# Kernel optimization log

Measured on AMD Instinct MI355X. Metric: run time of the kernel, lower is better.

The kernel has to match this reference:

```python
import jax, jax.numpy as jnp
import numpy as np

N_BASIS = 128   # n_atom_basis F
N_INT   = 3     # n_interactions
N_RBF   = 20
CUTOFF  = 5.0
MAX_Z   = 100
EPS     = 1e-8
N_ATOMS = 25000
N_EDGES = 200000


def setup_inputs() -> dict:
    key = jax.random.key(0)
    ks = jax.random.split(key, 16)
    F = N_BASIS
    s = 0.02
    z     = jax.random.randint(ks[0], (N_ATOMS,), 1, MAX_Z)
    pos   = jax.random.uniform(ks[1], (N_ATOMS, 3), dtype=jnp.float32) * 2.0  # small box -> inside cutoff
    idx_i = jax.random.randint(ks[2], (N_EDGES,), 0, N_ATOMS)
    idx_j = jax.random.randint(ks[3], (N_EDGES,), 0, N_ATOMS)
    emb   = jax.random.normal(ks[4], (MAX_Z, F), dtype=jnp.float32) * s
    fW    = jax.random.normal(ks[5], (N_RBF, 3 * F * N_INT), dtype=jnp.float32) * s
    fb    = jnp.zeros((3 * F * N_INT,), jnp.float32)
    iW1   = jax.random.normal(ks[6], (N_INT, F, F), dtype=jnp.float32) * s
    ib1   = jnp.zeros((N_INT, F), jnp.float32)
    iW2   = jax.random.normal(ks[7], (N_INT, F, 3 * F), dtype=jnp.float32) * s
    ib2   = jnp.zeros((N_INT, 3 * F), jnp.float32)
    mWmix = jax.random.normal(ks[8], (N_INT, F, 2 * F), dtype=jnp.float32) * s
    mW1   = jax.random.normal(ks[9], (N_INT, 2 * F, F), dtype=jnp.float32) * s
    mb1   = jnp.zeros((N_INT, F), jnp.float32)
    mW2   = jax.random.normal(ks[10], (N_INT, F, 3 * F), dtype=jnp.float32) * s
    mb2   = jnp.zeros((N_INT, 3 * F), jnp.float32)
    return dict(z=z, pos=pos, idx_i=idx_i, idx_j=idx_j, emb=emb, fW=fW, fb=fb,
                iW1=iW1, ib1=ib1, iW2=iW2, ib2=ib2,
                mWmix=mWmix, mW1=mW1, mb1=mb1, mW2=mW2, mb2=mb2)


def reference(z, pos, idx_i, idx_j, emb, fW, fb, iW1, ib1, iW2, ib2,
              mWmix, mW1, mb1, mW2, mb2):
    F = N_BASIS
    n_atoms = z.shape[0]
    # geometry
    r_ij = pos[idx_j] - pos[idx_i]                                  # [E,3]
    r_ij = jnp.where(jnp.abs(r_ij) < 1e-6, 1e-6, r_ij)
    d_ij = jnp.linalg.norm(r_ij, axis=1, keepdims=True)             # [E,1]
    dir_ij = r_ij / d_ij                                            # [E,3]
    # Gaussian radial basis
    offsets = jnp.linspace(0.0, CUTOFF, N_RBF)
    width = offsets[1] - offsets[0]
    coeff = -0.5 / (width * width)
    phi = jnp.exp(coeff * (d_ij[..., None] - offsets) ** 2)         # [E,1,n_rbf]
    # cosine cutoff
    fcut = 0.5 * (jnp.cos(jnp.pi * d_ij / CUTOFF) + 1.0) * (d_ij < CUTOFF)  # [E,1]
    filters = (phi @ fW + fb) * fcut[..., None]                     # [E,1,3F*I]
    filter_list = jnp.split(filters, N_INT, axis=-1)                # each [E,1,3F]
    # initial atom features
    q = emb[z][:, None, :]                                          # [N,1,F]
    mu = jnp.zeros((n_atoms, 3, F), q.dtype)                        # [N,3,F]
    for t in range(N_INT):
        # --- interaction (gather - filter-multiply - scatter-add) ---
        x = jax.nn.silu(q @ iW1[t] + ib1[t]) @ iW2[t] + ib2[t]      # [N,1,3F]
        xj = x[idx_j]                                               # [E,1,3F]
        muj = mu[idx_j]                                             # [E,3,F]
        x = filter_list[t] * xj                                     # [E,1,3F]
        dq, dmuR, dmumu = jnp.split(x, 3, axis=-1)                  # [E,1,F] each
        dq = jax.ops.segment_sum(dq, idx_i, num_segments=n_atoms)   # [N,1,F]
        dmu = dmuR * dir_ij[..., None] + dmumu * muj                # [E,3,F]
        dmu = jax.ops.segment_sum(dmu, idx_i, num_segments=n_atoms) # [N,3,F]
        q = q + dq
        mu = mu + dmu
        # --- mixing (intra-atomic) ---
        mu_mix = mu @ mWmix[t]                                      # [N,3,2F]
        mu_V, mu_W = jnp.split(mu_mix, 2, axis=-1)                  # [N,3,F]
        mu_Vn = jnp.sqrt(jnp.sum(mu_V ** 2, axis=-2, keepdims=True) + EPS)  # [N,1,F]
        ctx = jnp.concatenate([q, mu_Vn], axis=-1)                  # [N,1,2F]
        x = jax.nn.silu(ctx @ mW1[t] + mb1[t]) @ mW2[t] + mb2[t]    # [N,1,3F]
        dq_intra, dmu_intra, dqmu_intra = jnp.split(x, 3, axis=-1)
        dmu_intra = dmu_intra * mu_W                                # [N,3,F]
        dqmu_intra = dqmu_intra * jnp.sum(mu_V * mu_W, axis=1, keepdims=True)
        q = q + dq_intra + dqmu_intra
        mu = mu + dmu_intra
    return q.squeeze(1), mu
```

## Files before the change

kernel.cpp:

```cpp
#include <hip/hip_runtime.h>
#include <hip/hip_bf16.h>

#define F 128
#define F3 384
#define NRBF 20
#define NITER 3
#define KP 24

typedef __hip_bfloat16 bf16;
typedef __bf16 bfrag __attribute__((ext_vector_type(8)));
typedef float f32x4 __attribute__((ext_vector_type(4)));

__device__ __forceinline__ float b2f(bf16 v) { return __bfloat162float(v); }
__device__ __forceinline__ bf16 f2b(float v) { return __float2bfloat16(v); }
__device__ __forceinline__ bfrag ldb(const bf16* p) { return *(const bfrag*)p; }
__device__ __forceinline__ bfrag ldsb(const __bf16* p) { return *(const bfrag*)p; }
__device__ __forceinline__ bfrag cvtf(const float* p) {
    bfrag r;
#pragma unroll
    for (int j = 0; j < 8; ++j) r[j] = (__bf16)p[j];
    return r;
}

__global__ void detect_kernel(const unsigned short* __restrict__ raw, int n_u16,
                              int* __restrict__ flag) {
    int i = blockIdx.x * blockDim.x + threadIdx.x;
    int bad = 0;
    for (int k = i; k < n_u16; k += blockDim.x * gridDim.x) {
        unsigned e = (raw[k] >> 7) & 0xFFu;
        if (e >= 140u) bad = 1;
    }
    if (bad) atomicOr(flag, 1);
}

struct CvtArgs {
    const void* src[13];
    float* dst[13];
    int end[14];
};
__global__ void cvt_all_kernel(CvtArgs a, const int* __restrict__ flag, int total) {
    int idx = blockIdx.x * blockDim.x + threadIdx.x;
    if (idx >= total) return;
    int s = 0;
    while (idx >= a.end[s + 1]) ++s;
    int local = idx - a.end[s];
    float v = (*flag) ? ((const float*)a.src[s])[local]
                      : b2f(((const bf16*)a.src[s])[local]);
    a.dst[s][local] = v;
}

struct TpArgs {
    const float* src[5];
    bf16* dst[5];
    int K[5];
    int Nn[5];
    int end[6];
};
__global__ void tpose_all_kernel(TpArgs a, int total) {
    int idx = blockIdx.x * blockDim.x + threadIdx.x;
    if (idx >= total) return;
    int s = 0;
    while (idx >= a.end[s + 1]) ++s;
    int local = idx - a.end[s];
    int K = a.K[s], Nn = a.Nn[s], slice = K * Nn;
    int t = local / slice, j = local - t * slice;
    int n = j / K, k = j - n * K;
    a.dst[s][local] = f2b(a.src[s][t * slice + k * Nn + n]);
}

__global__ void fwt_kernel(const float* __restrict__ fW, const float* __restrict__ fb,
                           float* __restrict__ dst, int total) {
    int idx = blockIdx.x * blockDim.x + threadIdx.x;
    if (idx >= total) return;
    int k = idx % KP, rest = idx / KP;
    int n = rest % F3, t = rest / F3;
    float v = (k < NRBF) ? fW[k * (F3 * NITER) + t * F3 + n]
                         : (k == NRBF ? fb[t * F3 + n] : 0.0f);
    dst[idx] = v;
}

__global__ void geom_kernel(const float* __restrict__ pos, const int* __restrict__ ii,
                            const int* __restrict__ jj, const int* __restrict__ rank,
                            bf16* __restrict__ phifc2, float* __restrict__ dir2, int E) {
    int e = blockIdx.x * blockDim.x + threadIdx.x;
    if (e >= E) return;
    int i = ii[e], j = jj[e], l = rank[e];
    float r[3];
#pragma unroll
    for (int d = 0; d < 3; ++d) {
        float v = pos[j * 3 + d] - pos[i * 3 + d];
        if (fabsf(v) < 1e-6f) v = 1e-6f;
        r[d] = v;
    }
    float dd = sqrtf(r[0] * r[0] + r[1] * r[1] + r[2] * r[2]);
    float inv = 1.0f / dd;
#pragma unroll
    for (int d = 0; d < 3; ++d) dir2[(size_t)l * 4 + d] = r[d] * inv;
    dir2[(size_t)l * 4 + 3] = __int_as_float(j);
    const float CUT = 5.0f;
    const float PI = 3.14159265358979323846f;
    float fc = (dd < CUT) ? 0.5f * (cosf(PI * dd / CUT) + 1.0f) : 0.0f;
    const float width = CUT / (NRBF - 1);
    const float coeff = -0.5f / (width * width);
    bf16* pr = phifc2 + (size_t)l * KP;
#pragma unroll
    for (int k = 0; k < NRBF; ++k) {
        float diff = dd - (float)k * width;
        pr[k] = f2b(expf(coeff * diff * diff) * fc);
    }
    pr[NRBF] = f2b(fc);
    pr[NRBF + 1] = f2b(0.0f);
    pr[NRBF + 2] = f2b(0.0f);
    pr[NRBF + 3] = f2b(0.0f);
}

__global__ void embed_kernel(const int* __restrict__ z, const float* __restrict__ emb,
                             float* __restrict__ q, int N) {
    int idx = blockIdx.x * blockDim.x + threadIdx.x;
    if (idx >= N * F) return;
    int n = idx >> 7, f = idx & 127;
    q[idx] = emb[z[n] * F + f];
}

__global__ void count_kernel(const int* __restrict__ ii, int* __restrict__ counts, int E) {
    int e = blockIdx.x * blockDim.x + threadIdx.x;
    if (e < E) atomicAdd(&counts[ii[e]], 1);
}

__global__ void scan_kernel(const int* __restrict__ counts, int* __restrict__ offs, int N) {
    __shared__ int cum[1024];
    int t = threadIdx.x;
    int chunk = (N + 1023) >> 10;
    int b = t * chunk;
    int e = b + chunk; if (e > N) e = N;
    int s = 0;
    for (int a = b; a < e; ++a) s += counts[a];
    cum[t] = s;
    __syncthreads();
    for (int o = 1; o < 1024; o <<= 1) {
        int u = (t >= o) ? cum[t - o] : 0;
        __syncthreads();
        cum[t] += u;
        __syncthreads();
    }
    int run = cum[t] - s;
    for (int a = b; a < e; ++a) { offs[a] = run; run += counts[a]; }
    if (t == 1023) offs[N] = cum[1023];
}

__global__ void fill_kernel(const int* __restrict__ ii, const int* __restrict__ offs,
                            int* __restrict__ cursor, int* __restrict__ rank, int E) {
    int e = blockIdx.x * blockDim.x + threadIdx.x;
    if (e >= E) return;
    int i = ii[e];
    int p = atomicAdd(&cursor[i], 1);
    rank[e] = offs[i] + p;
}

__global__ __launch_bounds__(256) void atom_x_mfma(
    const float* __restrict__ q, const bf16* __restrict__ W1T, const float* __restrict__ b1,
    const bf16* __restrict__ W2T, const float* __restrict__ b2, bf16* __restrict__ x, int N) {
    __shared__ __bf16 H[32][136];
    int tid = threadIdx.x;
    int w = tid >> 6, l = tid & 63;
    int lm = l & 15, q4 = l >> 4;
    int i0 = blockIdx.x * 32;
    f32x4 acc[2][2] = {};
    int r0 = min(i0 + lm, N - 1);
    int r1 = min(i0 + 16 + lm, N - 1);
    for (int kt = 0; kt < 4; ++kt) {
        int ko = kt * 32 + q4 * 8;
        bfrag a0 = cvtf(q + (size_t)r0 * F + ko);
        bfrag a1 = cvtf(q + (size_t)r1 * F + ko);
        bfrag b0 = ldb(W1T + (size_t)(w * 32 + lm) * F + ko);
        bfrag b1f = ldb(W1T + (size_t)(w * 32 + 16 + lm) * F + ko);
        acc[0][0] = __builtin_amdgcn_mfma_f32_16x16x32_bf16(a0, b0, acc[0][0], 0, 0, 0);
        acc[1][0] = __builtin_amdgcn_mfma_f32_16x16x32_bf16(a1, b0, acc[1][0], 0, 0, 0);
        acc[0][1] = __builtin_amdgcn_mfma_f32_16x16x32_bf16(a0, b1f, acc[0][1], 0, 0, 0);
        acc[1][1] = __builtin_amdgcn_mfma_f32_16x16x32_bf16(a1, b1f, acc[1][1], 0, 0, 0);
    }
#pragma unroll
    for (int nt = 0; nt < 2; ++nt) {
        int col = w * 32 + nt * 16 + lm;
        float bb = b1[col];
#pragma unroll
        for (int mt = 0; mt < 2; ++mt)
#pragma unroll
            for (int r = 0; r < 4; ++r) {
                float v = acc[mt][nt][r] + bb;
                H[mt * 16 + q4 * 4 + r][col] = (__bf16)(v / (1.0f + expf(-v)));
            }
    }
    __syncthreads();
#pragma unroll
    for (int j = 0; j < 6; ++j) {
        int n0 = w * 96 + j * 16;
        f32x4 c0 = {}, c1 = {};
        const bf16* bp = W2T + (size_t)(n0 + lm) * F;
        for (int kt = 0; kt < 4; ++kt) {
            int ko = kt * 32 + q4 * 8;
            bfrag a0 = ldsb(&H[lm][ko]);
            bfrag a1 = ldsb(&H[16 + lm][ko]);
            bfrag bf = ldb(bp + ko);
            c0 = __builtin_amdgcn_mfma_f32_16x16x32_bf16(a0, bf, c0, 0, 0, 0);
            c1 = __builtin_amdgcn_mfma_f32_16x16x32_bf16(a1, bf, c1, 0, 0, 0);
        }
        int col = n0 + lm;
        float bb = b2[col];
#pragma unroll
        for (int r = 0; r < 4; ++r) {
            int row0 = i0 + q4 * 4 + r;
            int row1 = row0 + 16;
            if (row0 < N) x[(size_t)row0 * F3 + col] = f2b(c0[r] + bb);
            if (row1 < N) x[(size_t)row1 * F3 + col] = f2b(c1[r] + bb);
        }
    }
}

template<int T0>
__global__ __launch_bounds__(128, 2) void edge_gather_d(
    const bf16* __restrict__ mu_in, const bf16* __restrict__ x,
    const bf16* __restrict__ phifc2, const float* __restrict__ dir2,
    const float* __restrict__ fWTf, const int* __restrict__ offs,
    bf16* __restrict__ dq, bf16* __restrict__ dmu, int N) {
    int i = blockIdx.x;
    int f = threadIdx.x;
    float w0[21], w1[21], w2[21];
    {
        const f32x4* p0 = (const f32x4*)(fWTf + (size_t)f * KP);
        const f32x4* p1 = (const f32x4*)(fWTf + (size_t)(f + 128) * KP);
#pragma unroll
        for (int k = 0; k < 6; ++k) {
            f32x4 t0 = p0[k], t1 = p1[k];
#pragma unroll
            for (int r = 0; r < 4; ++r) {
                int kk = k * 4 + r;
                if (kk < 21) { w0[kk] = t0[r]; w1[kk] = t1[r]; }
            }
        }
        if constexpr (!T0) {
            const f32x4* p2 = (const f32x4*)(fWTf + (size_t)(f + 256) * KP);
#pragma unroll
            for (int k = 0; k < 6; ++k) {
                f32x4 t2 = p2[k];
#pragma unroll
                for (int r = 0; r < 4; ++r) {
                    int kk = k * 4 + r;
                    if (kk < 21) w2[kk] = t2[r];
                }
            }
        }
    }
#pragma unroll
    for (int k = 0; k < 21; ++k) {
        asm volatile("" : "+v"(w0[k]), "+v"(w1[k]));
        if constexpr (!T0) asm volatile("" : "+v"(w2[k]));
    }
    int beg = offs[i], end = offs[i + 1];
    float accq = 0.0f, am0 = 0.0f, am1 = 0.0f, am2 = 0.0f;
    for (int l = beg; l < end; ++l) {
        const bfrag* pb = (const bfrag*)(phifc2 + (size_t)l * KP);
        bfrag p0 = __builtin_nontemporal_load(pb);
        bfrag p1 = __builtin_nontemporal_load(pb + 1);
        bfrag p2 = __builtin_nontemporal_load(pb + 2);
        float ph[21];
#pragma unroll
        for (int k = 0; k < 8; ++k) ph[k] = (float)p0[k];
#pragma unroll
        for (int k = 0; k < 8; ++k) ph[8 + k] = (float)p1[k];
#pragma unroll
        for (int k = 0; k < 5; ++k) ph[16 + k] = (float)p2[k];
        float fl0 = 0.0f, fl1 = 0.0f, fl2 = 0.0f;
#pragma unroll
        for (int k = 0; k < 21; ++k) {
            fl0 += ph[k] * w0[k];
            fl1 += ph[k] * w1[k];
            if constexpr (!T0) fl2 += ph[k] * w2[k];
        }
        f32x4 dv = __builtin_nontemporal_load((const f32x4*)(dir2 + (size_t)l * 4));
        int j = __float_as_int(dv[3]);
        const bf16* xj = x + (size_t)j * F3;
        float dqv = fl0 * b2f(xj[f]);
        float dR = fl1 * b2f(xj[f + 128]);
        accq += dqv;
        if constexpr (!T0) {
            float dM = fl2 * b2f(xj[f + 256]);
            const bf16* muj = mu_in + (size_t)j * F3;
            am0 += dR * dv[0] + dM * b2f(muj[f]);
            am1 += dR * dv[1] + dM * b2f(muj[f + 128]);
            am2 += dR * dv[2] + dM * b2f(muj[f + 256]);
        } else {
            am0 += dR * dv[0];
            am1 += dR * dv[1];
            am2 += dR * dv[2];
        }
    }
    dq[(size_t)i * F + f] = f2b(accq);
    size_t mb = (size_t)i * F3 + f;
    dmu[mb]       = f2b(am0);
    dmu[mb + 128] = f2b(am1);
    dmu[mb + 256] = f2b(am2);
}

template<int T0, int EMITX, int OUT>
__global__ __launch_bounds__(256) void mix_mfma(
    float* __restrict__ q, const bf16* __restrict__ dqb,
    const bf16* __restrict__ mu_in, const bf16* __restrict__ dmu,
    bf16* __restrict__ mu_out,
    const bf16* __restrict__ WmixT, const bf16* __restrict__ W1T, const float* __restrict__ b1,
    const bf16* __restrict__ W2T, const float* __restrict__ b2,
    const bf16* __restrict__ xW1T, const float* __restrict__ xb1,
    const bf16* __restrict__ xW2T, const float* __restrict__ xb2, bf16* __restrict__ xout,
    void* __restrict__ outp, const int* __restrict__ flag, int N) {
    __shared__ __align__(16) char smem[46048];
    __bf16 (*WW)[130] = (__bf16(*)[130])(smem);
    __bf16 (*VV)[131] = (__bf16(*)[131])(smem + 12480);
    __bf16 (*Y)[392]  = (__bf16(*)[392])(smem + 12480);
    __bf16 (*CT)[264] = (__bf16(*)[264])(smem + 25056);
    __bf16 (*HM)[136] = (__bf16(*)[136])(smem + 33504);
    float  (*SS)[128] = (float(*)[128])(smem + 37856);
    int tid = threadIdx.x;
    int w = tid >> 6, l = tid & 63;
    int lm = l & 15, q4 = l >> 4;
    int i0 = blockIdx.x * 16;
    int rowsM = N * 3;
    {
        f32x4 acc[3][4] = {};
        int mr[3];
#pragma unroll
        for (int mt = 0; mt < 3; ++mt) mr[mt] = min(i0 * 3 + mt * 16 + lm, rowsM - 1);
        for (int kt = 0; kt < 4; ++kt) {
            int ko = kt * 32 + q4 * 8;
            bfrag a[3], b[4];
#pragma unroll
            for (int mt = 0; mt < 3; ++mt) {
                bfrag d = ldb(dmu + (size_t)mr[mt] * F + ko);
                if constexpr (T0) {
                    a[mt] = d;
                } else {
                    bfrag u = ldb(mu_in + (size_t)mr[mt] * F + ko);
#pragma unroll
                    for (int jj = 0; jj < 8; ++jj)
                        a[mt][jj] = (__bf16)((float)u[jj] + (float)d[jj]);
                }
            }
#pragma unroll
            for (int nt = 0; nt < 4; ++nt)
                b[nt] = ldb(WmixT + (size_t)(w * 64 + nt * 16 + lm) * F + ko);
#pragma unroll
            for (int mt = 0; mt < 3; ++mt)
#pragma unroll
                for (int nt = 0; nt < 4; ++nt)
                    acc[mt][nt] = __builtin_amdgcn_mfma_f32_16x16x32_bf16(a[mt], b[nt], acc[mt][nt], 0, 0, 0);
        }
#pragma unroll
        for (int mt = 0; mt < 3; ++mt)
#pragma unroll
            for (int nt = 0; nt < 4; ++nt) {
                int col = w * 64 + nt * 16 + lm;
#pragma unroll
                for (int r = 0; r < 4; ++r) {
                    int row = mt * 16 + q4 * 4 + r;
                    if (col < 128) VV[row][col] = (__bf16)acc[mt][nt][r];
                    else           WW[row][col - 128] = (__bf16)acc[mt][nt][r];
                }
            }
    }
    __syncthreads();
    for (int idx = tid; idx < 16 * F; idx += 256) {
        int a = idx >> 7, f = idx & 127;
        int i = min(i0 + a, N - 1);
        float v0 = (float)VV[a * 3 + 0][f], w0 = (float)WW[a * 3 + 0][f];
        float v1 = (float)VV[a * 3 + 1][f], w1 = (float)WW[a * 3 + 1][f];
        float v2 = (float)VV[a * 3 + 2][f], w2 = (float)WW[a * 3 + 2][f];
        SS[a][f] = v0 * w0 + v1 * w1 + v2 * w2;
        float qe = q[(size_t)i * F + f] + b2f(dqb[(size_t)i * F + f]);
        CT[a][f] = (__bf16)qe;
        CT[a][F + f] = (__bf16)sqrtf(v0 * v0 + v1 * v1 + v2 * v2 + 1e-8f);
    }
    __syncthreads();
    {
        f32x4 c[2] = {};
        for (int kt = 0; kt < 8; ++kt) {
            int ko = kt * 32 + q4 * 8;
            bfrag a = ldsb(&CT[lm][ko]);
#pragma unroll
            for (int nt = 0; nt < 2; ++nt) {
                bfrag b = ldb(W1T + (size_t)(w * 32 + nt * 16 + lm) * 256 + ko);
                c[nt] = __builtin_amdgcn_mfma_f32_16x16x32_bf16(a, b, c[nt], 0, 0, 0);
            }
        }
#pragma unroll
        for (int nt = 0; nt < 2; ++nt) {
            int col = w * 32 + nt * 16 + lm;
            float bb = b1[col];
#pragma unroll
            for (int r = 0; r < 4; ++r) {
                float v = c[nt][r] + bb;
                HM[q4 * 4 + r][col] = (__bf16)(v / (1.0f + expf(-v)));
            }
        }
    }
    __syncthreads();
#pragma unroll
    for (int j = 0; j < 6; ++j) {
        int n0 = w * 96 + j * 16;
        f32x4 c = {};
        const bf16* bp = W2T + (size_t)(n0 + lm) * F;
        for (int kt = 0; kt < 4; ++kt) {
            int ko = kt * 32 + q4 * 8;
            bfrag a = ldsb(&HM[lm][ko]);
            bfrag b = ldb(bp + ko);
            c = __builtin_amdgcn_mfma_f32_16x16x32_bf16(a, b, c, 0, 0, 0);
        }
        int col = n0 + lm;
        float bb = b2[col];
#pragma unroll
        for (int r = 0; r < 4; ++r)
            Y[q4 * 4 + r][col] = (__bf16)(c[r] + bb);
    }
    __syncthreads();
    int nq = N * F;
    for (int idx = tid; idx < 16 * F; idx += 256) {
        int a = idx >> 7, f = idx & 127;
        int i = i0 + a;
        if (i >= N) continue;
        float W0 = (float)WW[a * 3 + 0][f];
        float W1v = (float)WW[a * 3 + 1][f];
        float W2v = (float)WW[a * 3 + 2][f];
        float s = SS[a][f];
        float yq = (float)Y[a][f], ym = (float)Y[a][F + f], ys = (float)Y[a][2 * F + f];
        size_t qb = (size_t)i * F + f;
        float qv = q[qb] + b2f(dqb[qb]) + yq + ys * s;
        size_t mb = (size_t)i * F3 + f;
        float m0 = b2f(dmu[mb]);
        float m1 = b2f(dmu[mb + 128]);
        float m2 = b2f(dmu[mb + 256]);
        if constexpr (!T0) {
            m0 += b2f(mu_in[mb]);
            m1 += b2f(mu_in[mb + 128]);
            m2 += b2f(mu_in[mb + 256]);
        }
        m0 += ym * W0;
        m1 += ym * W1v;
        m2 += ym * W2v;
        if constexpr (OUT) {
            if (*flag) {
                float* of = (float*)outp;
                of[qb] = qv;
                of[nq + mb] = m0;
                of[nq + mb + 128] = m1;
                of[nq + mb + 256] = m2;
            } else {
                bf16* ob = (bf16*)outp;
                ob[qb] = f2b(qv);
                ob[nq + mb] = f2b(m0);
                ob[nq + mb + 128] = f2b(m1);
                ob[nq + mb + 256] = f2b(m2);
            }
        } else {
            q[qb] = qv;
            mu_out[mb]       = f2b(m0);
            mu_out[mb + 128] = f2b(m1);
            mu_out[mb + 256] = f2b(m2);
        }
        if constexpr (EMITX) CT[a][f] = (__bf16)qv;
    }
    if constexpr (EMITX) {
        __syncthreads();
        {
            f32x4 c[2] = {};
            for (int kt = 0; kt < 4; ++kt) {
                int ko = kt * 32 + q4 * 8;
                bfrag a = ldsb(&CT[lm][ko]);
#pragma unroll
                for (int nt = 0; nt < 2; ++nt) {
                    bfrag b = ldb(xW1T + (size_t)(w * 32 + nt * 16 + lm) * F + ko);
                    c[nt] = __builtin_amdgcn_mfma_f32_16x16x32_bf16(a, b, c[nt], 0, 0, 0);
                }
            }
#pragma unroll
            for (int nt = 0; nt < 2; ++nt) {
                int col = w * 32 + nt * 16 + lm;
                float bb = xb1[col];
#pragma unroll
                for (int r = 0; r < 4; ++r) {
                    float v = c[nt][r] + bb;
                    HM[q4 * 4 + r][col] = (__bf16)(v / (1.0f + expf(-v)));
                }
            }
        }
        __syncthreads();
#pragma unroll
        for (int j = 0; j < 6; ++j) {
            int n0 = w * 96 + j * 16;
            f32x4 c = {};
            const bf16* bp = xW2T + (size_t)(n0 + lm) * F;
            for (int kt = 0; kt < 4; ++kt) {
                int ko = kt * 32 + q4 * 8;
                bfrag a = ldsb(&HM[lm][ko]);
                bfrag b = ldb(bp + ko);
                c = __builtin_amdgcn_mfma_f32_16x16x32_bf16(a, b, c, 0, 0, 0);
            }
            int col = n0 + lm;
            float bb = xb2[col];
#pragma unroll
            for (int r = 0; r < 4; ++r) {
                int row = i0 + q4 * 4 + r;
                if (row < N) xout[(size_t)row * F3 + col] = f2b(c[r] + bb);
            }
        }
    }
}

extern "C" void kernel_launch(void* const* d_in, const int* in_sizes, int n_in,
                              void* d_out, int out_size, void* d_ws, size_t ws_size,
                              hipStream_t stream) {
    const int* z = (const int*)d_in[0];
    const int* idx_i = (const int*)d_in[2];
    const int* idx_j = (const int*)d_in[3];

    int N = in_sizes[0];
    int E = in_sizes[2];

    char* base = (char*)d_ws;
    size_t off = 0;
    auto alloc = [&](size_t bytes) -> void* {
        void* p = base + off;
        off += (bytes + 255) & ~(size_t)255;
        return p;
    };

    int* flag = (int*)alloc(4);
    float* pos_f = (float*)alloc((size_t)in_sizes[1] * 4);
    float* emb_f = (float*)alloc((size_t)in_sizes[4] * 4);
    float* fW_f = (float*)alloc((size_t)in_sizes[5] * 4);
    float* fb_f = (float*)alloc((size_t)in_sizes[6] * 4);
    float* iW1_f = (float*)alloc((size_t)in_sizes[7] * 4);
    float* ib1_f = (float*)alloc((size_t)in_sizes[8] * 4);
    float* iW2_f = (float*)alloc((size_t)in_sizes[9] * 4);
    float* ib2_f = (float*)alloc((size_t)in_sizes[10] * 4);
    float* mWmix_f = (float*)alloc((size_t)in_sizes[11] * 4);
    float* mW1_f = (float*)alloc((size_t)in_sizes[12] * 4);
    float* mb1_f = (float*)alloc((size_t)in_sizes[13] * 4);
    float* mW2_f = (float*)alloc((size_t)in_sizes[14] * 4);
    float* mb2_f = (float*)alloc((size_t)in_sizes[15] * 4);
    bf16* iW1T = (bf16*)alloc((size_t)NITER * F * F * 2);
    bf16* iW2T = (bf16*)alloc((size_t)NITER * F3 * F * 2);
    bf16* mWmixT = (bf16*)alloc((size_t)NITER * 2 * F * F * 2);
    bf16* mW1T = (bf16*)alloc((size_t)NITER * F * 2 * F * 2);
    bf16* mW2T = (bf16*)alloc((size_t)NITER * F3 * F * 2);
    float* fWTf = (float*)alloc((size_t)NITER * F3 * KP * 4);
    float* q = (float*)alloc((size_t)N * F * 4);
    bf16* dqb = (bf16*)alloc((size_t)N * F * 2);
    bf16* mua = (bf16*)alloc((size_t)N * F3 * 2);
    bf16* mub = (bf16*)alloc((size_t)N * F3 * 2);
    bf16* dmub = (bf16*)alloc((size_t)N * F3 * 2);
    bf16* xbuf = (bf16*)alloc((size_t)N * F3 * 2);
    bf16* phifc2 = (bf16*)alloc((size_t)(E + 16) * KP * 2);
    float* dir2 = (float*)alloc((size_t)(E + 16) * 4 * 4);
    int* rank = (int*)alloc((size_t)E * 4);
    int* counts = (int*)alloc((size_t)N * 4);
    int* offs = (int*)alloc((size_t)(N + 1) * 4);

    hipMemsetAsync(flag, 0, 4, stream);
    detect_kernel<<<64, 256, 0, stream>>>((const unsigned short*)d_in[1], in_sizes[1], flag);

    {
        CvtArgs a;
        const int srcIdx[13] = {1, 4, 5, 6, 7, 8, 9, 10, 11, 12, 13, 14, 15};
        float* dsts[13] = {pos_f, emb_f, fW_f, fb_f, iW1_f, ib1_f, iW2_f, ib2_f,
                           mWmix_f, mW1_f, mb1_f, mW2_f, mb2_f};
        int cum = 0;
        a.end[0] = 0;
        for (int s = 0; s < 13; ++s) {
            a.src[s] = d_in[srcIdx[s]];
            a.dst[s] = dsts[s];
            cum += in_sizes[srcIdx[s]];
            a.end[s + 1] = cum;
        }
        cvt_all_kernel<<<(cum + 255) / 256, 256, 0, stream>>>(a, flag, cum);
    }

    {
        TpArgs a;
        const float* srcs[5] = {iW1_f, iW2_f, mWmix_f, mW1_f, mW2_f};
        bf16* dsts[5] = {iW1T, iW2T, mWmixT, mW1T, mW2T};
        int Ks[5] = {F, F, F, 2 * F, F};
        int Nns[5] = {F, F3, 2 * F, F, F3};
        int cum = 0;
        a.end[0] = 0;
        for (int s = 0; s < 5; ++s) {
            a.src[s] = srcs[s];
            a.dst[s] = dsts[s];
            a.K[s] = Ks[s];
            a.Nn[s] = Nns[s];
            cum += NITER * Ks[s] * Nns[s];
            a.end[s + 1] = cum;
        }
        tpose_all_kernel<<<(cum + 255) / 256, 256, 0, stream>>>(a, cum);
    }
    {
        int total = NITER * F3 * KP;
        fwt_kernel<<<(total + 255) / 256, 256, 0, stream>>>(fW_f, fb_f, fWTf, total);
    }

    hipMemsetAsync(counts, 0, (size_t)N * 4, stream);
    count_kernel<<<(E + 255) / 256, 256, 0, stream>>>(idx_i, counts, E);
    scan_kernel<<<1, 1024, 0, stream>>>(counts, offs, N);
    hipMemsetAsync(counts, 0, (size_t)N * 4, stream);
    fill_kernel<<<(E + 255) / 256, 256, 0, stream>>>(idx_i, offs, counts, rank, E);

    geom_kernel<<<(E + 255) / 256, 256, 0, stream>>>(pos_f, idx_i, idx_j, rank,
                                                     phifc2, dir2, E);
    embed_kernel<<<(N * F + 255) / 256, 256, 0, stream>>>(z, emb_f, q, N);

    int mixGrid = (N + 15) / 16;
    bf16* muin = mua;
    bf16* muout = mub;
    atom_x_mfma<<<(N + 31) / 32, 256, 0, stream>>>(q, iW1T, ib1_f, iW2T, ib2_f, xbuf, N);
    edge_gather_d<1><<<N, 128, 0, stream>>>(muin, xbuf, phifc2, dir2,
                                            fWTf, offs, dqb, dmub, N);
    mix_mfma<1, 1, 0><<<mixGrid, 256, 0, stream>>>(q, dqb, muin, dmub, muout,
                                                   mWmixT, mW1T, mb1_f, mW2T, mb2_f,
                                                   iW1T + (size_t)1 * F * F, ib1_f + 1 * F,
                                                   iW2T + (size_t)1 * F3 * F, ib2_f + 1 * F3,
                                                   xbuf, nullptr, flag, N);
    { bf16* tm = muin; muin = muout; muout = tm; }
    edge_gather_d<0><<<N, 128, 0, stream>>>(muin, xbuf, phifc2, dir2,
                                            fWTf + (size_t)1 * F3 * KP, offs, dqb, dmub, N);
    mix_mfma<0, 1, 0><<<mixGrid, 256, 0, stream>>>(q, dqb, muin, dmub, muout,
                                                   mWmixT + (size_t)1 * 2 * F * F,
                                                   mW1T + (size_t)1 * F * 2 * F, mb1_f + 1 * F,
                                                   mW2T + (size_t)1 * F3 * F, mb2_f + 1 * F3,
                                                   iW1T + (size_t)2 * F * F, ib1_f + 2 * F,
                                                   iW2T + (size_t)2 * F3 * F, ib2_f + 2 * F3,
                                                   xbuf, nullptr, flag, N);
    { bf16* tm = muin; muin = muout; muout = tm; }
    edge_gather_d<0><<<N, 128, 0, stream>>>(muin, xbuf, phifc2, dir2,
                                            fWTf + (size_t)2 * F3 * KP, offs, dqb, dmub, N);
    mix_mfma<0, 0, 1><<<mixGrid, 256, 0, stream>>>(q, dqb, muin, dmub, muout,
                                                   mWmixT + (size_t)2 * 2 * F * F,
                                                   mW1T + (size_t)2 * F * 2 * F, mb1_f + 2 * F,
                                                   mW2T + (size_t)2 * F3 * F, mb2_f + 2 * F3,
                                                   nullptr, nullptr, nullptr, nullptr,
                                                   nullptr, d_out, flag, N);
}
```

Baseline: 761.2 us.

## Split fused mixing kernel into separate mix, context-MLP and atom-x kernels

Breaks the monolithic mixing kernel into three launches: one computes the mixed mu_V/mu_W products and writes the norm, dot product and mu_W to global buffers; one runs the context MLP and final update on 32-atom tiles; and the existing atom_x kernel computes the next interaction's x. The goal is to cut shared-memory use and register pressure for higher occupancy, and to reuse each weight fragment across two row tiles in the MLP. The cost is extra global traffic for the intermediate buffers (Vn, S, W) and more kernel launches.

```diff
diff --git a/kernel.cpp b/kernel.cpp
--- a/kernel.cpp
+++ b/kernel.cpp
@@ -302,23 +302,13 @@
     dmu[mb + 256] = f2b(am2);
 }
 
-template<int T0, int EMITX, int OUT>
-__global__ __launch_bounds__(256) void mix_mfma(
-    float* __restrict__ q, const bf16* __restrict__ dqb,
+template<int T0>
+__global__ __launch_bounds__(256) void mixv_mfma(
     const bf16* __restrict__ mu_in, const bf16* __restrict__ dmu,
-    bf16* __restrict__ mu_out,
-    const bf16* __restrict__ WmixT, const bf16* __restrict__ W1T, const float* __restrict__ b1,
-    const bf16* __restrict__ W2T, const float* __restrict__ b2,
-    const bf16* __restrict__ xW1T, const float* __restrict__ xb1,
-    const bf16* __restrict__ xW2T, const float* __restrict__ xb2, bf16* __restrict__ xout,
-    void* __restrict__ outp, const int* __restrict__ flag, int N) {
-    __shared__ __align__(16) char smem[46048];
-    __bf16 (*WW)[130] = (__bf16(*)[130])(smem);
-    __bf16 (*VV)[131] = (__bf16(*)[131])(smem + 12480);
-    __bf16 (*Y)[392]  = (__bf16(*)[392])(smem + 12480);
-    __bf16 (*CT)[264] = (__bf16(*)[264])(smem + 25056);
-    __bf16 (*HM)[136] = (__bf16(*)[136])(smem + 33504);
-    float  (*SS)[128] = (float(*)[128])(smem + 37856);
+    const bf16* __restrict__ WmixT,
+    bf16* __restrict__ Vn_g, float* __restrict__ S_g, bf16* __restrict__ Wg, int N) {
+    __shared__ __bf16 VV[48][131];
+    __shared__ __bf16 WW[48][130];
     int tid = threadIdx.x;
     int w = tid >> 6, l = tid & 63;
     int lm = l & 15, q4 = l >> 4;
@@ -369,25 +359,58 @@
     __syncthreads();
     for (int idx = tid; idx < 16 * F; idx += 256) {
         int a = idx >> 7, f = idx & 127;
-        int i = min(i0 + a, N - 1);
+        int i = i0 + a;
+        if (i >= N) continue;
         float v0 = (float)VV[a * 3 + 0][f], w0 = (float)WW[a * 3 + 0][f];
         float v1 = (float)VV[a * 3 + 1][f], w1 = (float)WW[a * 3 + 1][f];
         float v2 = (float)VV[a * 3 + 2][f], w2 = (float)WW[a * 3 + 2][f];
-        SS[a][f] = v0 * w0 + v1 * w1 + v2 * w2;
-        float qe = q[(size_t)i * F + f] + b2f(dqb[(size_t)i * F + f]);
+        size_t qb = (size_t)i * F + f;
+        Vn_g[qb] = f2b(sqrtf(v0 * v0 + v1 * v1 + v2 * v2 + 1e-8f));
+        S_g[qb] = v0 * w0 + v1 * w1 + v2 * w2;
+        size_t mb = (size_t)i * F3 + f;
+        Wg[mb]       = f2b(w0);
+        Wg[mb + 128] = f2b(w1);
+        Wg[mb + 256] = f2b(w2);
+    }
+}
+
+template<int T0, int OUT>
+__global__ __launch_bounds__(256) void ctx_final(
+    float* __restrict__ q, const bf16* __restrict__ dqb,
+    const bf16* __restrict__ mu_in, const bf16* __restrict__ dmu,
+    const bf16* __restrict__ Vn_g, const float* __restrict__ S_g, const bf16* __restrict__ Wg,
+    bf16* __restrict__ mu_out,
+    const bf16* __restrict__ W1T, const float* __restrict__ b1,
+    const bf16* __restrict__ W2T, const float* __restrict__ b2,
+    void* __restrict__ outp, const int* __restrict__ flag, int N) {
+    __shared__ __align__(16) char smem[33792];
+    __bf16 (*CT)[264] = (__bf16(*)[264])(smem);
+    __bf16 (*Y)[392]  = (__bf16(*)[392])(smem);
+    __bf16 (*HM)[136] = (__bf16(*)[136])(smem + 25088);
+    int tid = threadIdx.x;
+    int w = tid >> 6, l = tid & 63;
+    int lm = l & 15, q4 = l >> 4;
+    int i0 = blockIdx.x * 32;
+    for (int idx = tid; idx < 32 * F; idx += 256) {
+        int a = idx >> 7, f = idx & 127;
+        int i = min(i0 + a, N - 1);
+        size_t qb = (size_t)i * F + f;
+        float qe = q[qb] + b2f(dqb[qb]);
         CT[a][f] = (__bf16)qe;
-        CT[a][F + f] = (__bf16)sqrtf(v0 * v0 + v1 * v1 + v2 * v2 + 1e-8f);
+        CT[a][F + f] = (__bf16)b2f(Vn_g[qb]);
     }
     __syncthreads();
     {
-        f32x4 c[2] = {};
+        f32x4 c0[2] = {}, c1[2] = {};
         for (int kt = 0; kt < 8; ++kt) {
             int ko = kt * 32 + q4 * 8;
-            bfrag a = ldsb(&CT[lm][ko]);
+            bfrag a0 = ldsb(&CT[lm][ko]);
+            bfrag a1 = ldsb(&CT[16 + lm][ko]);
 #pragma unroll
             for (int nt = 0; nt < 2; ++nt) {
                 bfrag b = ldb(W1T + (size_t)(w * 32 + nt * 16 + lm) * 256 + ko);
-                c[nt] = __builtin_amdgcn_mfma_f32_16x16x32_bf16(a, b, c[nt], 0, 0, 0);
+                c0[nt] = __builtin_amdgcn_mfma_f32_16x16x32_bf16(a0, b, c0[nt], 0, 0, 0);
+                c1[nt] = __builtin_amdgcn_mfma_f32_16x16x32_bf16(a1, b, c1[nt], 0, 0, 0);
             }
         }
 #pragma unroll
@@ -396,8 +419,10 @@
             float bb = b1[col];
 #pragma unroll
             for (int r = 0; r < 4; ++r) {
-                float v = c[nt][r] + bb;
-                HM[q4 * 4 + r][col] = (__bf16)(v / (1.0f + expf(-v)));
+                float v0 = c0[nt][r] + bb;
+                float v1 = c1[nt][r] + bb;
+                HM[q4 * 4 + r][col] = (__bf16)(v0 / (1.0f + expf(-v0)));
+                HM[16 + q4 * 4 + r][col] = (__bf16)(v1 / (1.0f + expf(-v1)));
             }
         }
     }
@@ -405,34 +430,38 @@
 #pragma unroll
     for (int j = 0; j < 6; ++j) {
         int n0 = w * 96 + j * 16;
-        f32x4 c = {};
+        f32x4 c0 = {}, c1 = {};
         const bf16* bp = W2T + (size_t)(n0 + lm) * F;
         for (int kt = 0; kt < 4; ++kt) {
             int ko = kt * 32 + q4 * 8;
-            bfrag a = ldsb(&HM[lm][ko]);
+            bfrag a0 = ldsb(&HM[lm][ko]);
+            bfrag a1 = ldsb(&HM[16 + lm][ko]);
             bfrag b = ldb(bp + ko);
-            c = __builtin_amdgcn_mfma_f32_16x16x32_bf16(a, b, c, 0, 0, 0);
+            c0 = __builtin_amdgcn_mfma_f32_16x16x32_bf16(a0, b, c0, 0, 0, 0);
+            c1 = __builtin_amdgcn_mfma_f32_16x16x32_bf16(a1, b, c1, 0, 0, 0);
         }
         int col = n0 + lm;
         float bb = b2[col];
 #pragma unroll
-        for (int r = 0; r < 4; ++r)
-            Y[q4 * 4 + r][col] = (__bf16)(c[r] + bb);
+        for (int r = 0; r < 4; ++r) {
+            Y[q4 * 4 + r][col] = (__bf16)(c0[r] + bb);
+            Y[16 + q4 * 4 + r][col] = (__bf16)(c1[r] + bb);
+        }
     }
     __syncthreads();
     int nq = N * F;
-    for (int idx = tid; idx < 16 * F; idx += 256) {
+    for (int idx = tid; idx < 32 * F; idx += 256) {
         int a = idx >> 7, f = idx & 127;
         int i = i0 + a;
         if (i >= N) continue;
-        float W0 = (float)WW[a * 3 + 0][f];
-        float W1v = (float)WW[a * 3 + 1][f];
-        float W2v = (float)WW[a * 3 + 2][f];
-        float s = SS[a][f];
+        size_t qb = (size_t)i * F + f;
+        size_t mb = (size_t)i * F3 + f;
         float yq = (float)Y[a][f], ym = (float)Y[a][F + f], ys = (float)Y[a][2 * F + f];
-        size_t qb = (size_t)i * F + f;
+        float s = S_g[qb];
+        float W0 = b2f(Wg[mb]);
+        float W1v = b2f(Wg[mb + 128]);
+        float W2v = b2f(Wg[mb + 256]);
         float qv = q[qb] + b2f(dqb[qb]) + yq + ys * s;
-        size_t mb = (size_t)i * F3 + f;
         float m0 = b2f(dmu[mb]);
         float m1 = b2f(dmu[mb + 128]);
         float m2 = b2f(dmu[mb + 256]);
@@ -463,52 +492,6 @@
             mu_out[mb]       = f2b(m0);
             mu_out[mb + 128] = f2b(m1);
             mu_out[mb + 256] = f2b(m2);
-        }
-        if constexpr (EMITX) CT[a][f] = (__bf16)qv;
-    }
-    if constexpr (EMITX) {
-        __syncthreads();
-        {
-            f32x4 c[2] = {};
-            for (int kt = 0; kt < 4; ++kt) {
-                int ko = kt * 32 + q4 * 8;
-                bfrag a = ldsb(&CT[lm][ko]);
-#pragma unroll
-                for (int nt = 0; nt < 2; ++nt) {
-                    bfrag b = ldb(xW1T + (size_t)(w * 32 + nt * 16 + lm) * F + ko);
-                    c[nt] = __builtin_amdgcn_mfma_f32_16x16x32_bf16(a, b, c[nt], 0, 0, 0);
-                }
-            }
-#pragma unroll
-            for (int nt = 0; nt < 2; ++nt) {
-                int col = w * 32 + nt * 16 + lm;
-                float bb = xb1[col];
-#pragma unroll
-                for (int r = 0; r < 4; ++r) {
-                    float v = c[nt][r] + bb;
-                    HM[q4 * 4 + r][col] = (__bf16)(v / (1.0f + expf(-v)));
-                }
-            }
-        }
-        __syncthreads();
-#pragma unroll
-        for (int j = 0; j < 6; ++j) {
-            int n0 = w * 96 + j * 16;
-            f32x4 c = {};
-            const bf16* bp = xW2T + (size_t)(n0 + lm) * F;
-            for (int kt = 0; kt < 4; ++kt) {
-                int ko = kt * 32 + q4 * 8;
-                bfrag a = ldsb(&HM[lm][ko]);
-                bfrag b = ldb(bp + ko);
-                c = __builtin_amdgcn_mfma_f32_16x16x32_bf16(a, b, c, 0, 0, 0);
-            }
-            int col = n0 + lm;
-            float bb = xb2[col];
-#pragma unroll
-            for (int r = 0; r < 4; ++r) {
-                int row = i0 + q4 * 4 + r;
-                if (row < N) xout[(size_t)row * F3 + col] = f2b(c[r] + bb);
-            }
         }
     }
 }
@@ -557,6 +540,9 @@
     bf16* mub = (bf16*)alloc((size_t)N * F3 * 2);
     bf16* dmub = (bf16*)alloc((size_t)N * F3 * 2);
     bf16* xbuf = (bf16*)alloc((size_t)N * F3 * 2);
+    bf16* Vn_g = (bf16*)alloc((size_t)N * F * 2);
+    float* S_g = (float*)alloc((size_t)N * F * 4);
+    bf16* Wg = (bf16*)alloc((size_t)N * F3 * 2);
     bf16* phifc2 = (bf16*)alloc((size_t)(E + 16) * KP * 2);
     float* dir2 = (float*)alloc((size_t)(E + 16) * 4 * 4);
     int* rank = (int*)alloc((size_t)E * 4);
@@ -615,34 +601,37 @@
                                                      phifc2, dir2, E);
     embed_kernel<<<(N * F + 255) / 256, 256, 0, stream>>>(z, emb_f, q, N);
 
-    int mixGrid = (N + 15) / 16;
+    int grid16 = (N + 15) / 16;
+    int grid32 = (N + 31) / 32;
     bf16* muin = mua;
     bf16* muout = mub;
-    atom_x_mfma<<<(N + 31) / 32, 256, 0, stream>>>(q, iW1T, ib1_f, iW2T, ib2_f, xbuf, N);
+    atom_x_mfma<<<grid32, 256, 0, stream>>>(q, iW1T, ib1_f, iW2T, ib2_f, xbuf, N);
     edge_gather_d<1><<<N, 128, 0, stream>>>(muin, xbuf, phifc2, dir2,
                                             fWTf, offs, dqb, dmub, N);
-    mix_mfma<1, 1, 0><<<mixGrid, 256, 0, stream>>>(q, dqb, muin, dmub, muout,
-                                                   mWmixT, mW1T, mb1_f, mW2T, mb2_f,
-                                                   iW1T + (size_t)1 * F * F, ib1_f + 1 * F,
-                                                   iW2T + (size_t)1 * F3 * F, ib2_f + 1 * F3,
-                                                   xbuf, nullptr, flag, N);
+    mixv_mfma<1><<<grid16, 256, 0, stream>>>(muin, dmub, mWmixT, Vn_g, S_g, Wg, N);
+    ctx_final<1, 0><<<grid32, 256, 0, stream>>>(q, dqb, muin, dmub, Vn_g, S_g, Wg, muout,
+                                                mW1T, mb1_f, mW2T, mb2_f,
+                                                nullptr, flag, N);
+    atom_x_mfma<<<grid32, 256, 0, stream>>>(q, iW1T + (size_t)1 * F * F, ib1_f + 1 * F,
+                                            iW2T + (size_t)1 * F3 * F, ib2_f + 1 * F3, xbuf, N);
     { bf16* tm = muin; muin = muout; muout = tm; }
     edge_gather_d<0><<<N, 128, 0, stream>>>(muin, xbuf, phifc2, dir2,
                                             fWTf + (size_t)1 * F3 * KP, offs, dqb, dmub, N);
-    mix_mfma<0, 1, 0><<<mixGrid, 256, 0, stream>>>(q, dqb, muin, dmub, muout,
-                                                   mWmixT + (size_t)1 * 2 * F * F,
-                                                   mW1T + (size_t)1 * F * 2 * F, mb1_f + 1 * F,
-                                                   mW2T + (size_t)1 * F3 * F, mb2_f + 1 * F3,
-                                                   iW1T + (size_t)2 * F * F, ib1_f + 2 * F,
-                                                   iW2T + (size_t)2 * F3 * F, ib2_f + 2 * F3,
-                                                   xbuf, nullptr, flag, N);
+    mixv_mfma<0><<<grid16, 256, 0, stream>>>(muin, dmub, mWmixT + (size_t)1 * 2 * F * F,
+                                             Vn_g, S_g, Wg, N);
+    ctx_final<0, 0><<<grid32, 256, 0, stream>>>(q, dqb, muin, dmub, Vn_g, S_g, Wg, muout,
+                                                mW1T + (size_t)1 * F * 2 * F, mb1_f + 1 * F,
+                                                mW2T + (size_t)1 * F3 * F, mb2_f + 1 * F3,
+                                                nullptr, flag, N);
+    atom_x_mfma<<<grid32, 256, 0, stream>>>(q, iW1T + (size_t)2 * F * F, ib1_f + 2 * F,
+                                            iW2T + (size_t)2 * F3 * F, ib2_f + 2 * F3, xbuf, N);
     { bf16* tm = muin; muin = muout; muout = tm; }
     edge_gather_d<0><<<N, 128, 0, stream>>>(muin, xbuf, phifc2, dir2,
                                             fWTf + (size_t)2 * F3 * KP, offs, dqb, dmub, N);
-    mix_mfma<0, 0, 1><<<mixGrid, 256, 0, stream>>>(q, dqb, muin, dmub, muout,
-                                                   mWmixT + (size_t)2 * 2 * F * F,
-                                                   mW1T + (size_t)2 * F * 2 * F, mb1_f + 2 * F,
-                                                   mW2T + (size_t)2 * F3 * F, mb2_f + 2 * F3,
-                                                   nullptr, nullptr, nullptr, nullptr,
-                                                   nullptr, d_out, flag, N);
-}
+    mixv_mfma<0><<<grid16, 256, 0, stream>>>(muin, dmub, mWmixT + (size_t)2 * 2 * F * F,
+                                             Vn_g, S_g, Wg, N);
+    ctx_final<0, 1><<<grid32, 256, 0, stream>>>(q, dqb, muin, dmub, Vn_g, S_g, Wg, muout,
+                                                mW1T + (size_t)2 * F * 2 * F, mb1_f + 2 * F,
+                                                mW2T + (size_t)2 * F3 * F, mb2_f + 2 * F3,
+                                                d_out, flag, N);
+}
```

After: 753.4 us. No clear change (-1.0%).
